# Kernel optimization log

Hardware: AMD Instinct MI355X
Metric: run time of the kernel (lower is better)

Reference implementation:

```python
import jax, jax.numpy as jnp
import numpy as np

N, E, C_IN = 100000, 800000, 128


def setup_inputs() -> dict:
    key = jax.random.key(0)
    ks = jax.random.split(key, 16)
    x = jax.random.normal(ks[0], (N, C_IN), dtype=jnp.float32)
    edge_index = jax.random.randint(ks[1], (2, E), 0, N, dtype=jnp.int64)

    def glorot(k, shape):
        lim = float(np.sqrt(6.0 / (shape[0] + shape[1])))
        return jax.random.uniform(k, shape, jnp.float32, -lim, lim)

    # channels = [128, 128, 256, 256, 256, 112]; layers 0,3 are l_GCN, layers 1,2,4 are l_SAGE
    params = dict(
        alpha=0.1 * jax.random.normal(ks[2], (5,), jnp.float32),  # ReZero alphas (init'd !=0 to exercise path)
        W0=glorot(ks[3], (128, 128)), b0=jnp.zeros((128,), jnp.float32),
        W1=glorot(ks[4], (128, 256)), R1=glorot(ks[5], (128, 256)), b1=jnp.zeros((256,), jnp.float32),
        W2=glorot(ks[6], (256, 256)), R2=glorot(ks[7], (256, 256)), b2=jnp.zeros((256,), jnp.float32),
        W3=glorot(ks[8], (256, 256)), b3=jnp.zeros((256,), jnp.float32),
        W4=glorot(ks[9], (256, 112)), R4=glorot(ks[10], (256, 112)), b4=jnp.zeros((112,), jnp.float32),
    )
    return dict(x=x, edge_index=edge_index, **params)


def reference(x, edge_index, alpha, W0, b0, W1, R1, b1, W2, R2, b2, W3, b3, W4, R4, b4):
    n = x.shape[0]
    row, col = edge_index[0], edge_index[1]
    ones = jnp.ones((row.shape[0],), x.dtype)
    deg = jax.ops.segment_sum(ones, row, num_segments=n)        # out-degree per node
    dinv = jnp.where(deg > 0, jax.lax.rsqrt(jnp.maximum(deg, 1e-12)), 0.0)
    cnt = jnp.maximum(deg, 1.0)[:, None]                        # mean-aggregation denominator

    def gcn_agg(h):  # D^-1/2 A D^-1/2 @ h
        m = h[col] * dinv[col][:, None]                          # [E, C] gather + scale
        return jax.ops.segment_sum(m, row, num_segments=n) * dinv[:, None]

    def mean_agg(h):  # SparseTensor.matmul(h, reduce='mean')
        return jax.ops.segment_sum(h[col], row, num_segments=n) / cnt

    # layer 0: l_GCN, re_list, rezero=1 -> residual from y[0]; dropout = identity (eval)
    t0 = gcn_agg(x) @ W0 + b0
    h = x + alpha[0] * t0
    # layer 1: l_SAGE + relu
    h = jax.nn.relu(mean_agg(h) @ W1 + h @ R1 + b1)
    # layer 2: l_SAGE + relu
    h = jax.nn.relu(mean_agg(h) @ W2 + h @ R2 + b2)
    # layer 3: l_GCN, re_list, rezero=1 -> residual from y[3] (current h)
    t3 = gcn_agg(h) @ W3 + b3
    h = h + alpha[3] * t3
    # layer 4: l_SAGE, no relu, no residual
    h = mean_agg(h) @ W4 + h @ R4 + b4
    return h
```

## Files before the change

### kernel.cpp

```cpp
#include <hip/hip_runtime.h>


typedef _Float16 __attribute__((ext_vector_type(8))) f16x8;
typedef _Float16 __attribute__((ext_vector_type(2))) f16x2;
typedef __attribute__((ext_vector_type(4))) float f32x4;

__device__ __forceinline__ unsigned short f2h(float f) {
    union { _Float16 h; unsigned short u; } v; v.h = (_Float16)f; return v.u;
}
__device__ __forceinline__ float h2f(unsigned short u) {
    union { unsigned short u; _Float16 h; } v; v.u = u; return (float)v.h;
}


__global__ __launch_bounds__(256) void zero_int_kernel(int* __restrict__ p, int n)
{
    int i = blockIdx.x * 256 + threadIdx.x;
    if (i < n) p[i] = 0;
}

__global__ __launch_bounds__(256) void count_deg_kernel(
    const int* __restrict__ row, int* __restrict__ deg, int E)
{
    int e = blockIdx.x * 256 + threadIdx.x;
    if (e < E) atomicAdd(&deg[row[e]], 1);
}

__global__ __launch_bounds__(1024) void scan_p1_kernel(
    const int* __restrict__ deg, int* __restrict__ rp,
    int* __restrict__ bsum, int n)
{
    __shared__ int wsum[16];
    int t = threadIdx.x, lane = t & 63, w = t >> 6;
    int base = blockIdx.x * 2048;
    int carry = 0;
    #pragma unroll
    for (int half = 0; half < 2; ++half) {
        int i = base + half * 1024 + t;
        int xv = (i < n) ? deg[i] : 0;
        int s = xv;
        #pragma unroll
        for (int off = 1; off < 64; off <<= 1) {
            int v = __shfl_up(s, off, 64);
            if (lane >= off) s += v;
        }
        if (lane == 63) wsum[w] = s;
        __syncthreads();
        if (w == 0 && lane < 16) {
            int ws = wsum[lane];
            #pragma unroll
            for (int off = 1; off < 16; off <<= 1) {
                int v = __shfl_up(ws, off, 64);
                if (lane >= off) ws += v;
            }
            wsum[lane] = ws;
        }
        __syncthreads();
        int wo = (w == 0) ? 0 : wsum[w - 1];
        if (i < n) rp[i + 1] = carry + wo + s;
        carry += wsum[15];
        if (half == 0) __syncthreads();
    }
    if (t == 0) bsum[blockIdx.x] = carry;
}

__global__ __launch_bounds__(64) void scan_p2_kernel(int* __restrict__ bsum, int B)
{
    int lane = threadIdx.x;
    int v = (lane < B) ? bsum[lane] : 0;
    int s = v;
    #pragma unroll
    for (int off = 1; off < 64; off <<= 1) {
        int u = __shfl_up(s, off, 64);
        if (lane >= off) s += u;
    }
    if (lane < B) bsum[lane] = s - v;
}

__global__ __launch_bounds__(1024) void scan_p3_kernel(
    const int* __restrict__ deg, int* __restrict__ rp,
    int* __restrict__ cursor, const int* __restrict__ bsum,
    float* __restrict__ dinv, float* __restrict__ cinv, int n)
{
    int boff = bsum[blockIdx.x];
    int base = blockIdx.x * 2048;
    #pragma unroll
    for (int half = 0; half < 2; ++half) {
        int i = base + half * 1024 + threadIdx.x;
        if (i < n) {
            int d = deg[i];
            int incl = rp[i + 1] + boff;
            rp[i + 1] = incl;
            cursor[i] = incl - d;
            float df = (float)d;
            dinv[i] = (d > 0) ? rsqrtf(df) : 0.0f;
            cinv[i] = 1.0f / fmaxf(df, 1.0f);
        }
    }
    if (blockIdx.x == 0 && threadIdx.x == 0) rp[0] = 0;
}

__global__ __launch_bounds__(256) void fill_csr_kernel(
    const int* __restrict__ row, const int* __restrict__ col,
    int* __restrict__ cursor, int* __restrict__ colS, int E)
{
    int e = blockIdx.x * 256 + threadIdx.x;
    if (e < E) {
        int p = atomicAdd(&cursor[row[e]], 1);
        colS[p] = col[e];
    }
}


__global__ __launch_bounds__(256) void f32_to_f16_kernel(
    const float* __restrict__ src, unsigned short* __restrict__ dst, int n4)
{
    int i = blockIdx.x * 256 + threadIdx.x;
    if (i >= n4) return;
    float4 v = ((const float4*)src)[i];
    ushort4 o;
    o.x = f2h(v.x); o.y = f2h(v.y); o.z = f2h(v.z); o.w = f2h(v.w);
    ((ushort4*)dst)[i] = o;
}

__global__ __launch_bounds__(256) void prep_w_kernel(
    const float* __restrict__ S1, int K1,
    const float* __restrict__ S2, int K2,
    int Nout, int Npad, unsigned short* __restrict__ dst)
{
    int Ktot = K1 + K2;
    int idx = blockIdx.x * 256 + threadIdx.x;
    if (idx >= Npad * Ktot) return;
    int n = idx / Ktot, k = idx - n * Ktot;
    float v = 0.0f;
    if (n < Nout)
        v = (k < K1) ? S1[(size_t)k * Nout + n] : S2[(size_t)(k - K1) * Nout + n];
    dst[idx] = f2h(v);
}

__global__ __launch_bounds__(256) void prep_w2_kernel(
    const float* __restrict__ W4, const float* __restrict__ R4,
    unsigned short* __restrict__ dst)
{
    int idx = blockIdx.x * 256 + threadIdx.x;
    int nrow = idx >> 8, k = idx & 255;
    float v = 0.0f;
    if (nrow < 112)      v = W4[(size_t)k * 112 + nrow];
    else if (nrow < 224) v = R4[(size_t)k * 112 + (nrow - 112)];
    dst[idx] = f2h(v);
}

__global__ __launch_bounds__(256) void prep_biasP_kernel(
    const float* __restrict__ b4, float* __restrict__ biasP)
{
    int i = threadIdx.x;
    biasP[i] = (i >= 112 && i < 224) ? b4[i - 112] : 0.0f;
}


template <int C, bool HAS_ES, int OUT_MODE>
__global__ __launch_bounds__(256) void agg_f16_kernel(
    const unsigned short* __restrict__ h, int ldh,
    const int* __restrict__ rp, const int* __restrict__ cols,
    const float* __restrict__ escale, const float* __restrict__ nscale,
    unsigned short* __restrict__ out, int ldo,
    float* __restrict__ fout, int ldof, int n)
{
    constexpr int LPE = (C == 256) ? 32 : 16;
    constexpr int EPG = 64 / LPE;
    constexpr int UNR = 4;
    int node = blockIdx.x * 4 + (threadIdx.x >> 6);
    if (node >= n) return;
    int lane = threadIdx.x & 63;
    int grp = lane / LPE, sub = lane % LPE;
    const unsigned short* hc = h + sub * 8;

    int s = rp[node], e = rp[node + 1];
    const _Float16 hz = (_Float16)0.0f;
    f16x2 zz = { hz, hz };
    f16x2 acc2[4];
    #pragma unroll
    for (int k = 0; k < 4; ++k) acc2[k] = zz;

    for (int i = s; i < e; i += UNR * EPG) {
        int cc[UNR]; f16x2 ssv[UNR]; uint4 uu[UNR];
        #pragma unroll
        for (int u = 0; u < UNR; ++u) {
            int ii = i + u * EPG + grp;
            bool valid = ii < e;
            int c = valid ? cols[ii] : 0;
            cc[u] = c;
            float sc = valid ? (HAS_ES ? escale[c] : 1.0f) : 0.0f;
            _Float16 sh = (_Float16)sc;
            f16x2 sv = { sh, sh };
            ssv[u] = sv;
        }
        #pragma unroll
        for (int u = 0; u < UNR; ++u)
            uu[u] = *(const uint4*)(hc + (size_t)cc[u] * ldh);
        #pragma unroll
        for (int u = 0; u < UNR; ++u) {
            union { uint4 q; f16x2 hh[4]; } cv; cv.q = uu[u];
            #pragma unroll
            for (int p = 0; p < 4; ++p)
                acc2[p] += cv.hh[p] * ssv[u];
        }
    }

    #pragma unroll
    for (int k = 0; k < 4; ++k) {
        union { f16x2 h2; float f; } a, b;
        a.h2 = acc2[k];
        if (EPG == 4) { b.f = __shfl_xor(a.f, 16, 64); a.h2 = a.h2 + b.h2; }
        b.f = __shfl_xor(a.f, 32, 64); a.h2 = a.h2 + b.h2;
        acc2[k] = a.h2;
    }

    if (OUT_MODE == 0) {
        if (grp == 0) {
            _Float16 nh = (_Float16)nscale[node];
            f16x2 nn = { nh, nh };
            union { uint4 q; f16x2 hh[4]; } o;
            #pragma unroll
            for (int p = 0; p < 4; ++p) o.hh[p] = acc2[p] * nn;
            *(uint4*)(out + (size_t)node * ldo + sub * 8) = o.q;
        }
    } else {
        if (grp == 0 && sub < 14) {
            float cs = nscale[node];
            float* U = fout + (size_t)node * ldof + sub * 8;
            float4 u0 = *(float4*)U;
            float4 u1 = *(float4*)(U + 4);
            u0.x += cs * (float)acc2[0][0];
            u0.y += cs * (float)acc2[0][1];
            u0.z += cs * (float)acc2[1][0];
            u0.w += cs * (float)acc2[1][1];
            u1.x += cs * (float)acc2[2][0];
            u1.y += cs * (float)acc2[2][1];
            u1.z += cs * (float)acc2[3][0];
            u1.w += cs * (float)acc2[3][1];
            *(float4*)U = u0;
            *(float4*)(U + 4) = u1;
        }
    }
}


__device__ __forceinline__ void g2l16(const unsigned short* g, unsigned short* l) {
    __builtin_amdgcn_global_load_lds(
        (const __attribute__((address_space(1))) unsigned int*)g,
        (__attribute__((address_space(3))) unsigned int*)l, 16, 0, 0);
}

template <int BN, int EPI, bool RES_F16, bool WF32, bool WB16>
__global__ __launch_bounds__(2 * BN) void mfma_gemm_kernel(
    const unsigned short* __restrict__ A1, int K1, int lda1,
    const unsigned short* __restrict__ A2, int K2, int lda2,
    const unsigned short* __restrict__ Bt,
    const float* __restrict__ bias,
    const void* __restrict__ res, int ldres,
    const float* __restrict__ alpha_ptr, int alpha_idx,
    float* __restrict__ outf, unsigned short* __restrict__ outb, int ldo,
    int M, int Nout)
{
    constexpr int WAVES = BN / 32;
    constexpr int AI = 256 / BN;
    constexpr int L  = AI + 2;
    __shared__ unsigned short As[3][128 * 32];
    __shared__ unsigned short Bs[3][BN * 32];
    int t = threadIdx.x;
    int m0 = blockIdx.x * 128, n0 = blockIdx.y * BN;
    int Ktot = K1 + K2;
    int w = t >> 6, lane = t & 63;
    int wm = w & 1, wn = w >> 1;
    int q = lane >> 4, l16 = lane & 15;

    int koff = (((lane & 3) ^ ((lane >> 2) & 3)) * 8);
    int rsub = lane >> 2;

    f32x4 acc[4][4];
    #pragma unroll
    for (int i = 0; i < 4; ++i)
        #pragma unroll
        for (int j = 0; j < 4; ++j)
            #pragma unroll
            for (int r = 0; r < 4; ++r) acc[i][j][r] = 0.0f;

    const int KC = Ktot >> 5;

    auto issue = [&](int kc, int p) {
        int k0 = kc * 32;
        const unsigned short* Ap; int lda, kk;
        if (k0 < K1) { Ap = A1; lda = lda1; kk = k0; }
        else         { Ap = A2; lda = lda2; kk = k0 - K1; }
        #pragma unroll
        for (int a = 0; a < AI; ++a) {
            int rb = a * 16 * WAVES + w * 16;
            int gm = m0 + rb + rsub; if (gm >= M) gm = M - 1;
            g2l16(Ap + (size_t)gm * lda + kk + koff, &As[p][rb * 32]);
        }
        #pragma unroll
        for (int b = 0; b < 2; ++b) {
            int rb = b * 16 * WAVES + w * 16;
            int gn = n0 + rb + rsub;
            g2l16(Bt + (size_t)gn * Ktot + k0 + koff, &Bs[p][rb * 32]);
        }
    };

    const int cq = (q ^ (l16 & 3)) * 8;
    const int rbA = (wm * 64 + l16) * 32 + cq;
    const int rbB = (wn * 64 + l16) * 32 + cq;

    issue(0, 0);
    if (KC > 1) issue(1, 1);
    if (KC > 2) issue(2, 2);

    int p = 0;
    for (int kc = 0; kc < KC; ++kc) {
        int rem = KC - 1 - kc;
        if (rem >= 2) {
            if constexpr (L == 4) asm volatile("s_waitcnt vmcnt(8)" ::: "memory");
            else                  asm volatile("s_waitcnt vmcnt(6)" ::: "memory");
        } else if (rem == 1) {
            if constexpr (L == 4) asm volatile("s_waitcnt vmcnt(4)" ::: "memory");
            else                  asm volatile("s_waitcnt vmcnt(3)" ::: "memory");
        } else {
            asm volatile("s_waitcnt vmcnt(0)" ::: "memory");
        }
        __builtin_amdgcn_s_barrier();
        asm volatile("" ::: "memory");

        f16x8 af[4], bfr[4];
        #pragma unroll
        for (int i = 0; i < 4; ++i)
            af[i] = *(const f16x8*)&As[p][rbA + i * 16 * 32];
        #pragma unroll
        for (int j = 0; j < 4; ++j)
            bfr[j] = *(const f16x8*)&Bs[p][rbB + j * 16 * 32];

        asm volatile("s_waitcnt lgkmcnt(0)" ::: "memory");
        __builtin_amdgcn_s_barrier();
        asm volatile("" ::: "memory");
        if (kc + 3 < KC) issue(kc + 3, p);

        __builtin_amdgcn_s_setprio(1);
        #pragma unroll
        for (int i = 0; i < 4; ++i)
            #pragma unroll
            for (int j = 0; j < 4; ++j)
                acc[i][j] = __builtin_amdgcn_mfma_f32_16x16x32_f16(
                    bfr[j], af[i], acc[i][j], 0, 0, 0);
        __builtin_amdgcn_s_setprio(0);

        p = (p == 2) ? 0 : p + 1;
    }

    float alpha = 0.0f;
    if (EPI == 2) alpha = alpha_ptr[alpha_idx];
    #pragma unroll
    for (int i = 0; i < 4; ++i) {
        int m = m0 + wm * 64 + i * 16 + l16;
        if (m >= M) continue;
        #pragma unroll
        for (int j = 0; j < 4; ++j) {
            int nb = n0 + wn * 64 + j * 16 + q * 4;
            if (nb >= Nout) continue;
            float4 bv = *(const float4*)&bias[nb];
            float v0 = acc[i][j][0] + bv.x;
            float v1 = acc[i][j][1] + bv.y;
            float v2 = acc[i][j][2] + bv.z;
            float v3 = acc[i][j][3] + bv.w;
            if (EPI == 3) {
                if (nb < 112) {
                    *(ushort4*)&outb[(size_t)m * ldo + nb] =
                        make_ushort4(f2h(v0), f2h(v1), f2h(v2), f2h(v3));
                } else {
                    *(float4*)&outf[(size_t)m * ldres + (nb - 112)] =
                        make_float4(v0, v1, v2, v3);
                }
                continue;
            }
            if (EPI == 1) {
                v0 = fmaxf(v0, 0.0f); v1 = fmaxf(v1, 0.0f);
                v2 = fmaxf(v2, 0.0f); v3 = fmaxf(v3, 0.0f);
            }
            if (EPI == 2) {
                if (RES_F16) {
                    ushort4 rr = *(const ushort4*)
                        ((const unsigned short*)res + (size_t)m * ldres + nb);
                    v0 = h2f(rr.x) + alpha * v0;
                    v1 = h2f(rr.y) + alpha * v1;
                    v2 = h2f(rr.z) + alpha * v2;
                    v3 = h2f(rr.w) + alpha * v3;
                } else {
                    float4 rr = *(const float4*)
                        ((const float*)res + (size_t)m * ldres + nb);
                    v0 = rr.x + alpha * v0;
                    v1 = rr.y + alpha * v1;
                    v2 = rr.z + alpha * v2;
                    v3 = rr.w + alpha * v3;
                }
            }
            if (WF32) {
                *(float4*)&outf[(size_t)m * ldo + nb] = make_float4(v0, v1, v2, v3);
            }
            if (WB16) {
                *(ushort4*)&outb[(size_t)m * ldo + nb] =
                    make_ushort4(f2h(v0), f2h(v1), f2h(v2), f2h(v3));
            }
        }
    }
}


extern "C" void kernel_launch(void* const* d_in, const int* in_sizes, int n_in,
                              void* d_out, int out_size, void* d_ws, size_t ws_size,
                              hipStream_t stream)
{
    const float* x      = (const float*)d_in[0];
    const int*   ei     = (const int*)d_in[1];
    const float* alpha  = (const float*)d_in[2];
    const float* W0     = (const float*)d_in[3];
    const float* b0     = (const float*)d_in[4];
    const float* W1     = (const float*)d_in[5];
    const float* R1     = (const float*)d_in[6];
    const float* b1     = (const float*)d_in[7];
    const float* W2     = (const float*)d_in[8];
    const float* R2     = (const float*)d_in[9];
    const float* b2     = (const float*)d_in[10];
    const float* W3     = (const float*)d_in[11];
    const float* b3     = (const float*)d_in[12];
    const float* W4     = (const float*)d_in[13];
    const float* R4     = (const float*)d_in[14];
    const float* b4     = (const float*)d_in[15];

    const int N = in_sizes[0] / 128;
    const int E = in_sizes[1] / 2;
    const int* row = ei;
    const int* col = ei + E;

    size_t off = 0;
    auto alloc = [&](size_t bytes) -> void* {
        void* p = (char*)d_ws + off;
        off += (bytes + 255) & ~(size_t)255;
        return p;
    };
    int*   deg    = (int*)alloc((size_t)N * 4);
    int*   rp     = (int*)alloc((size_t)(N + 1) * 4);
    int*   cursor = (int*)alloc((size_t)N * 4);
    int*   colS   = (int*)alloc((size_t)E * 4);
    int*   bsum   = (int*)alloc((size_t)64 * 4);
    float* dinv   = (float*)alloc((size_t)N * 4);
    float* cinv   = (float*)alloc((size_t)N * 4);
    unsigned short* Wt0 = (unsigned short*)alloc((size_t)128 * 128 * 2);
    unsigned short* Wt1 = (unsigned short*)alloc((size_t)256 * 256 * 2);
    unsigned short* Wt2 = (unsigned short*)alloc((size_t)256 * 512 * 2);
    unsigned short* Wt3 = (unsigned short*)alloc((size_t)256 * 256 * 2);
    unsigned short* Wt4p= (unsigned short*)alloc((size_t)256 * 256 * 2);
    float* biasP  = (float*)alloc((size_t)256 * 4);
    unsigned short* Xb  = (unsigned short*)alloc((size_t)N * 128 * 2);
    unsigned short* Gb  = (unsigned short*)alloc((size_t)N * 256 * 2);
    unsigned short* Pb  = (unsigned short*)alloc((size_t)N * 256 * 2);
    unsigned short* Ab  = (unsigned short*)alloc((size_t)N * 256 * 2);
    unsigned short* Hb  = Xb;
    (void)ws_size;

    const int SB = (N + 2047) / 2048;
    zero_int_kernel<<<(N + 255) / 256, 256, 0, stream>>>(deg, N);
    count_deg_kernel<<<(E + 255) / 256, 256, 0, stream>>>(row, deg, E);
    scan_p1_kernel<<<SB, 1024, 0, stream>>>(deg, rp, bsum, N);
    scan_p2_kernel<<<1, 64, 0, stream>>>(bsum, SB);
    scan_p3_kernel<<<SB, 1024, 0, stream>>>(deg, rp, cursor, bsum, dinv, cinv, N);
    fill_csr_kernel<<<(E + 255) / 256, 256, 0, stream>>>(row, col, cursor, colS, E);

    f32_to_f16_kernel<<<(N * 32 + 255) / 256, 256, 0, stream>>>(x, Xb, N * 32);
    prep_w_kernel<<<(128 * 128 + 255) / 256, 256, 0, stream>>>(W0, 128, nullptr, 0, 128, 128, Wt0);
    prep_w_kernel<<<(256 * 256 + 255) / 256, 256, 0, stream>>>(W1, 128, R1, 128, 256, 256, Wt1);
    prep_w_kernel<<<(256 * 512 + 255) / 256, 256, 0, stream>>>(W2, 256, R2, 256, 256, 256, Wt2);
    prep_w_kernel<<<(256 * 256 + 255) / 256, 256, 0, stream>>>(W3, 256, nullptr, 0, 256, 256, Wt3);
    prep_w2_kernel<<<(256 * 256) / 256, 256, 0, stream>>>(W4, R4, Wt4p);
    prep_biasP_kernel<<<1, 256, 0, stream>>>(b4, biasP);

    dim3 aggGrid((N + 3) / 4);
    dim3 g1((N + 127) / 128, 1);

    agg_f16_kernel<128, true, 0><<<aggGrid, 256, 0, stream>>>(
        Xb, 128, rp, colS, dinv, dinv, Ab, 128, nullptr, 0, N);
    mfma_gemm_kernel<128, 2, false, false, true><<<g1, 256, 0, stream>>>(
        Ab, 128, 128, nullptr, 0, 0, Wt0, b0, x, 128, alpha, 0,
        nullptr, Hb, 128, N, 128);

    agg_f16_kernel<128, false, 0><<<aggGrid, 256, 0, stream>>>(
        Hb, 128, rp, colS, nullptr, cinv, Ab, 128, nullptr, 0, N);
    mfma_gemm_kernel<256, 1, false, false, true><<<g1, 512, 0, stream>>>(
        Ab, 128, 128, Hb, 128, 128, Wt1, b1, nullptr, 0, nullptr, 0,
        nullptr, Gb, 256, N, 256);

    agg_f16_kernel<256, false, 0><<<aggGrid, 256, 0, stream>>>(
        Gb, 256, rp, colS, nullptr, cinv, Ab, 256, nullptr, 0, N);
    mfma_gemm_kernel<256, 1, false, false, true><<<g1, 512, 0, stream>>>(
        Ab, 256, 256, Gb, 256, 256, Wt2, b2, nullptr, 0, nullptr, 0,
        nullptr, Pb, 256, N, 256);

    agg_f16_kernel<256, true, 0><<<aggGrid, 256, 0, stream>>>(
        Pb, 256, rp, colS, dinv, dinv, Ab, 256, nullptr, 0, N);
    mfma_gemm_kernel<256, 2, true, false, true><<<g1, 512, 0, stream>>>(
        Ab, 256, 256, nullptr, 0, 0, Wt3, b3, Pb, 256, alpha, 3,
        nullptr, Gb, 256, N, 256);

    mfma_gemm_kernel<256, 3, false, false, false><<<g1, 512, 0, stream>>>(
        Gb, 256, 256, nullptr, 0, 0, Wt4p, biasP, nullptr, 112, nullptr, 0,
        (float*)d_out, Ab, 128, N, 224);
    agg_f16_kernel<128, false, 1><<<aggGrid, 256, 0, stream>>>(
        Ab, 128, rp, colS, nullptr, cinv, nullptr, 0, (float*)d_out, 112, N);
}
```

Before: 675.4 us.

## Double GEMM M-tile to 256 rows with doubled waves per block

The MFMA GEMM block tile grows from 128 to 256 rows, and the thread count per block doubles (4*BN). The global-to-LDS load mapping, LDS swizzle, vmcnt wait counts and launch grid are reworked to match. The aim is to reuse each B tile across more rows and halve the number of blocks, cutting weight-load traffic and per-block overhead. In exchange it uses more LDS per block, and the larger blocks may lower occupancy or leave fewer blocks to balance across CUs.

```diff
diff --git a/kernel.cpp b/kernel.cpp
--- a/kernel.cpp
+++ b/kernel.cpp
@@ -253,7 +253,7 @@
 }
 
 template <int BN, int EPI, bool RES_F16, bool WF32, bool WB16>
-__global__ __launch_bounds__(2 * BN) void mfma_gemm_kernel(
+__global__ __launch_bounds__(4 * BN) void mfma_gemm_kernel(
     const unsigned short* __restrict__ A1, int K1, int lda1,
     const unsigned short* __restrict__ A2, int K2, int lda2,
     const unsigned short* __restrict__ Bt,
@@ -263,20 +263,21 @@
     float* __restrict__ outf, unsigned short* __restrict__ outb, int ldo,
     int M, int Nout)
 {
-    constexpr int WAVES = BN / 32;
-    constexpr int AI = 256 / BN;
-    constexpr int L  = AI + 2;
-    __shared__ unsigned short As[3][128 * 32];
+    constexpr int THREADS = 4 * BN;
+    constexpr int AI = (BN == 256) ? 1 : 2;
+    constexpr int L  = AI + 1;
+    constexpr int RPP = THREADS / 4;
+    __shared__ unsigned short As[3][256 * 32];
     __shared__ unsigned short Bs[3][BN * 32];
     int t = threadIdx.x;
-    int m0 = blockIdx.x * 128, n0 = blockIdx.y * BN;
+    int m0 = blockIdx.x * 256, n0 = blockIdx.y * BN;
     int Ktot = K1 + K2;
     int w = t >> 6, lane = t & 63;
-    int wm = w & 1, wn = w >> 1;
+    int wm = w & 3, wn = w >> 2;
     int q = lane >> 4, l16 = lane & 15;
 
-    int koff = (((lane & 3) ^ ((lane >> 2) & 3)) * 8);
-    int rsub = lane >> 2;
+    int koff = (((t & 3) ^ ((t >> 3) & 3)) * 8);
+    int rsub = t >> 2;
 
     f32x4 acc[4][4];
     #pragma unroll
@@ -295,19 +296,17 @@
         else         { Ap = A2; lda = lda2; kk = k0 - K1; }
         #pragma unroll
         for (int a = 0; a < AI; ++a) {
-            int rb = a * 16 * WAVES + w * 16;
-            int gm = m0 + rb + rsub; if (gm >= M) gm = M - 1;
-            g2l16(Ap + (size_t)gm * lda + kk + koff, &As[p][rb * 32]);
-        }
-        #pragma unroll
-        for (int b = 0; b < 2; ++b) {
-            int rb = b * 16 * WAVES + w * 16;
-            int gn = n0 + rb + rsub;
-            g2l16(Bt + (size_t)gn * Ktot + k0 + koff, &Bs[p][rb * 32]);
+            int gm = m0 + a * RPP + rsub; if (gm >= M) gm = M - 1;
+            g2l16(Ap + (size_t)gm * lda + kk + koff,
+                  &As[p][a * (RPP * 32) + w * 512]);
+        }
+        {
+            int gn = n0 + rsub;
+            g2l16(Bt + (size_t)gn * Ktot + k0 + koff, &Bs[p][w * 512]);
         }
     };
 
-    const int cq = (q ^ (l16 & 3)) * 8;
+    const int cq = (q ^ ((l16 >> 1) & 3)) * 8;
     const int rbA = (wm * 64 + l16) * 32 + cq;
     const int rbB = (wn * 64 + l16) * 32 + cq;
 
@@ -319,11 +318,11 @@
     for (int kc = 0; kc < KC; ++kc) {
         int rem = KC - 1 - kc;
         if (rem >= 2) {
-            if constexpr (L == 4) asm volatile("s_waitcnt vmcnt(8)" ::: "memory");
-            else                  asm volatile("s_waitcnt vmcnt(6)" ::: "memory");
+            if constexpr (L == 3) asm volatile("s_waitcnt vmcnt(6)" ::: "memory");
+            else                  asm volatile("s_waitcnt vmcnt(4)" ::: "memory");
         } else if (rem == 1) {
-            if constexpr (L == 4) asm volatile("s_waitcnt vmcnt(4)" ::: "memory");
-            else                  asm volatile("s_waitcnt vmcnt(3)" ::: "memory");
+            if constexpr (L == 3) asm volatile("s_waitcnt vmcnt(3)" ::: "memory");
+            else                  asm volatile("s_waitcnt vmcnt(2)" ::: "memory");
         } else {
             asm volatile("s_waitcnt vmcnt(0)" ::: "memory");
         }
@@ -333,10 +332,10 @@
         f16x8 af[4], bfr[4];
         #pragma unroll
         for (int i = 0; i < 4; ++i)
-            af[i] = *(const f16x8*)&As[p][rbA + i * 16 * 32];
+            af[i] = *(const f16x8*)&As[p][rbA + i * 512];
         #pragma unroll
         for (int j = 0; j < 4; ++j)
-            bfr[j] = *(const f16x8*)&Bs[p][rbB + j * 16 * 32];
+            bfr[j] = *(const f16x8*)&Bs[p][rbB + j * 512];
 
         asm volatile("s_waitcnt lgkmcnt(0)" ::: "memory");
         __builtin_amdgcn_s_barrier();
@@ -482,33 +481,33 @@
     prep_biasP_kernel<<<1, 256, 0, stream>>>(b4, biasP);
 
     dim3 aggGrid((N + 3) / 4);
-    dim3 g1((N + 127) / 128, 1);
+    dim3 gM((N + 255) / 256, 1);
 
     agg_f16_kernel<128, true, 0><<<aggGrid, 256, 0, stream>>>(
         Xb, 128, rp, colS, dinv, dinv, Ab, 128, nullptr, 0, N);
-    mfma_gemm_kernel<128, 2, false, false, true><<<g1, 256, 0, stream>>>(
+    mfma_gemm_kernel<128, 2, false, false, true><<<gM, 512, 0, stream>>>(
         Ab, 128, 128, nullptr, 0, 0, Wt0, b0, x, 128, alpha, 0,
         nullptr, Hb, 128, N, 128);
 
     agg_f16_kernel<128, false, 0><<<aggGrid, 256, 0, stream>>>(
         Hb, 128, rp, colS, nullptr, cinv, Ab, 128, nullptr, 0, N);
-    mfma_gemm_kernel<256, 1, false, false, true><<<g1, 512, 0, stream>>>(
+    mfma_gemm_kernel<256, 1, false, false, true><<<gM, 1024, 0, stream>>>(
         Ab, 128, 128, Hb, 128, 128, Wt1, b1, nullptr, 0, nullptr, 0,
         nullptr, Gb, 256, N, 256);
 
     agg_f16_kernel<256, false, 0><<<aggGrid, 256, 0, stream>>>(
         Gb, 256, rp, colS, nullptr, cinv, Ab, 256, nullptr, 0, N);
-    mfma_gemm_kernel<256, 1, false, false, true><<<g1, 512, 0, stream>>>(
+    mfma_gemm_kernel<256, 1, false, false, true><<<gM, 1024, 0, stream>>>(
         Ab, 256, 256, Gb, 256, 256, Wt2, b2, nullptr, 0, nullptr, 0,
         nullptr, Pb, 256, N, 256);
 
     agg_f16_kernel<256, true, 0><<<aggGrid, 256, 0, stream>>>(
         Pb, 256, rp, colS, dinv, dinv, Ab, 256, nullptr, 0, N);
-    mfma_gemm_kernel<256, 2, true, false, true><<<g1, 512, 0, stream>>>(
+    mfma_gemm_kernel<256, 2, true, false, true><<<gM, 1024, 0, stream>>>(
         Ab, 256, 256, nullptr, 0, 0, Wt3, b3, Pb, 256, alpha, 3,
         nullptr, Gb, 256, N, 256);
 
-    mfma_gemm_kernel<256, 3, false, false, false><<<g1, 512, 0, stream>>>(
+    mfma_gemm_kernel<256, 3, false, false, false><<<gM, 1024, 0, stream>>>(
         Gb, 256, 256, nullptr, 0, 0, Wt4p, biasP, nullptr, 112, nullptr, 0,
         (float*)d_out, Ab, 128, N, 224);
     agg_f16_kernel<128, false, 1><<<aggGrid, 256, 0, stream>>>(
```

Result: slower. 696.6 us (+3.1%).
